# Optimization experiments

Hardware: AMD Instinct MI355X
Metric: run time of the kernel (lower is better)

Reference implementation:

```python
import jax, jax.numpy as jnp
import numpy as np

NUM_HEADS = 16
KERNEL_SIZE = 13  # odd, neighborhood size nh = 6


def setup_inputs() -> dict:
    key = jax.random.key(0)
    ks = jax.random.split(key, 6)
    B, L, C = 4, 4096, 512
    return {
        "x": jax.random.normal(ks[0], (B, L, C), dtype=jnp.float32),
        "qkv_w": jax.random.normal(ks[1], (3 * C, C), dtype=jnp.float32) * (C ** -0.5),
        "qkv_b": jax.random.normal(ks[2], (3 * C,), dtype=jnp.float32) * 0.02,
        "rpb": jax.random.normal(ks[3], (NUM_HEADS, 2 * KERNEL_SIZE - 1), dtype=jnp.float32) * 0.02,
        "proj_w": jax.random.normal(ks[4], (C, C), dtype=jnp.float32) * (C ** -0.5),
        "proj_b": jax.random.normal(ks[5], (C,), dtype=jnp.float32) * 0.02,
    }


def reference(x, qkv_w, qkv_b, rpb, proj_w, proj_b):
    B, L, C = x.shape
    H, K = NUM_HEADS, KERNEL_SIZE
    Dh = C // H
    scale = Dh ** -0.5
    nh = K // 2

    # qkv projection (torch Linear: x @ W.T + b)
    qkv = (x @ qkv_w.T + qkv_b).reshape(B, L, 3, H, Dh)
    qkv = jnp.transpose(qkv, (2, 0, 3, 1, 4))  # (3, B, H, L, Dh)
    q, k, v = qkv[0] * scale, qkv[1], qkv[2]

    # neighborhood indices: window of K keys, shifted (not clipped) at borders
    pos = jnp.arange(L)
    start = jnp.clip(pos - nh, 0, L - K)            # (L,)
    idx = start[:, None] + jnp.arange(K)[None, :]   # (L, K) key positions
    # relative-position-bias index: (key_pos - query_pos) + (K-1), in [0, 2K-2]
    bias_idx = idx - pos[:, None] + (K - 1)         # (L, K)

    k_g = k[:, :, idx, :]                           # (B, H, L, K, Dh)
    attn = jnp.einsum('bhld,bhlkd->bhlk', q, k_g)   # (B, H, L, K)
    attn = attn + rpb[:, bias_idx][None]            # add (H, L, K) bias
    attn = jax.nn.softmax(attn, axis=-1)

    v_g = v[:, :, idx, :]                           # (B, H, L, K, Dh)
    out = jnp.einsum('bhlk,bhlkd->bhld', attn, v_g)  # (B, H, L, Dh)
    out = jnp.transpose(out, (0, 2, 1, 3)).reshape(B, L, C)
    return out @ proj_w.T + proj_b
```

## Files before the change

### kernel.cpp

```cpp
#include <hip/hip_runtime.h>
#include <hip/hip_bf16.h>

#define BATCH   4
#define LSEQ    4096
#define CCH     512
#define HNUM    16
#define DH      32
#define KSZ     13
#define NHALF   6
#define M_TOT   16384
#define N_QKV   1536
#define KDIM    512
#define BK      64

typedef __attribute__((ext_vector_type(8))) short  short8;
typedef __attribute__((ext_vector_type(4))) short  short4_t;
typedef __attribute__((ext_vector_type(4))) float  float4_t;

__device__ __forceinline__ unsigned short f32_to_bf16(float f) {
    union { float f; unsigned int u; } un; un.f = f;
    unsigned int u = un.u;
    u += 0x7FFFu + ((u >> 16) & 1u);
    return (unsigned short)(u >> 16);
}
__device__ __forceinline__ float bf16_to_f32(unsigned short h) {
    union { unsigned int u; float f; } un; un.u = ((unsigned int)h) << 16;
    return un.f;
}

__device__ __forceinline__ void gload_lds16(const unsigned short* g, unsigned short* l) {
    __builtin_amdgcn_global_load_lds(
        (const __attribute__((address_space(1))) unsigned int*)g,
        (__attribute__((address_space(3))) unsigned int*)l,
        16, 0, 0);
}

__global__ void cvt_f32_bf16_v4(const float4_t* __restrict__ in,
                                short4_t* __restrict__ out, int n4) {
    int i = blockIdx.x * blockDim.x + threadIdx.x;
    int stride = gridDim.x * blockDim.x;
    for (; i < n4; i += stride) {
        float4_t v = in[i];
        short4_t h;
        h.x = (short)f32_to_bf16(v.x);
        h.y = (short)f32_to_bf16(v.y);
        h.z = (short)f32_to_bf16(v.z);
        h.w = (short)f32_to_bf16(v.w);
        out[i] = h;
    }
}

__global__ __launch_bounds__(256) void gemm_qkv(
    const unsigned short* __restrict__ Xb,
    const unsigned short* __restrict__ W,
    const float* __restrict__ bias,
    unsigned short* __restrict__ qkvout)
{
    __shared__ __align__(16) unsigned short As[128 * BK];
    __shared__ __align__(16) unsigned short Bs[128 * BK];
    const int tid  = threadIdx.x;
    const int wv   = tid >> 6, ln = tid & 63;
    const int m0   = blockIdx.x * 128;
    const int n0   = blockIdx.y * 128;
    const int wm   = (wv >> 1) * 64;
    const int wn   = (wv & 1) * 64;
    const int lr   = ln & 15;
    const int lg   = ln >> 4;
    const int rgrp = ln >> 3;
    const int csw  = ((ln & 7) ^ rgrp) * 8;

    float4_t acc[4][4];
    #pragma unroll
    for (int m = 0; m < 4; ++m)
        #pragma unroll
        for (int n = 0; n < 4; ++n)
            acc[m][n] = (float4_t){0.f, 0.f, 0.f, 0.f};

    for (int k0 = 0; k0 < KDIM; k0 += BK) {
        #pragma unroll
        for (int it = 0; it < 4; ++it) {
            int ch  = it * 4 + wv;
            int row = ch * 8 + rgrp;
            gload_lds16(Xb + (size_t)(m0 + row) * KDIM + k0 + csw,
                        &As[ch * 8 * BK]);
            gload_lds16(W  + (size_t)(n0 + row) * KDIM + k0 + csw,
                        &Bs[ch * 8 * BK]);
        }
        __syncthreads();
        short8 af[2][4], bfr[2][4];
        #pragma unroll
        for (int kk = 0; kk < 2; ++kk) {
            #pragma unroll
            for (int m = 0; m < 4; ++m) {
                int row = wm + m * 16 + lr;
                int c   = (kk * 4 + lg) ^ (row & 7);
                af[kk][m] = *reinterpret_cast<const short8*>(&As[row * BK + c * 8]);
            }
            #pragma unroll
            for (int n = 0; n < 4; ++n) {
                int row = wn + n * 16 + lr;
                int c   = (kk * 4 + lg) ^ (row & 7);
                bfr[kk][n] = *reinterpret_cast<const short8*>(&Bs[row * BK + c * 8]);
            }
        }
        #pragma unroll
        for (int kk = 0; kk < 2; ++kk)
            #pragma unroll
            for (int m = 0; m < 4; ++m)
                #pragma unroll
                for (int n = 0; n < 4; ++n)
                    acc[m][n] = __builtin_amdgcn_mfma_f32_16x16x32_bf16(
                        af[kk][m], bfr[kk][n], acc[m][n], 0, 0, 0);
        __syncthreads();
    }

    const float qscale = 0.17677669529663687f;
    #pragma unroll
    for (int m = 0; m < 4; ++m) {
        #pragma unroll
        for (int n = 0; n < 4; ++n) {
            int gn    = n0 + wn + n * 16 + lr;
            int which = gn >> 9;
            int hh    = (gn >> 5) & 15;
            int dd    = gn & 31;
            float bsv = bias[gn];
            #pragma unroll
            for (int r = 0; r < 4; ++r) {
                int gm = m0 + wm + m * 16 + lg * 4 + r;
                float v = acc[m][n][r] + bsv;
                if (which == 0) v *= qscale;
                int b_ = gm >> 12, l = gm & 4095;
                size_t off = (((size_t)which * BATCH + b_) * HNUM + hh) *
                                 ((size_t)LSEQ * DH) + (size_t)l * DH + dd;
                qkvout[off] = f32_to_bf16(v);
            }
        }
    }
}

__global__ __launch_bounds__(256) void natten_fwd(
    const unsigned short* __restrict__ qkv,
    const float* __restrict__ rpb,
    unsigned short* __restrict__ ctx)
{
    __shared__ unsigned short ks[268 * DH];
    __shared__ unsigned short vs[268 * DH];
    __shared__ float rpb_s[2 * KSZ - 1];

    const int t    = threadIdx.x;
    const int lblk = blockIdx.x & 15;
    const int bh   = blockIdx.x >> 4;
    const int hh   = bh & 15, b_ = bh >> 4;
    const int l0   = lblk * 256;

    const int r0    = max(l0 - NHALF, 0);
    const int rend  = min(l0 + 256 + NHALF, LSEQ);
    const int nrows = rend - r0;

    const size_t plane = (size_t)LSEQ * DH;
    const size_t kbase = (((size_t)1 * BATCH + b_) * HNUM + hh) * plane;
    const size_t vbase = (((size_t)2 * BATCH + b_) * HNUM + hh) * plane;

    for (int slot = t; slot < nrows * 4; slot += 256) {
        int row = slot >> 2, cq = slot & 3;
        *reinterpret_cast<short8*>(&ks[row * DH + cq * 8]) =
            *reinterpret_cast<const short8*>(&qkv[kbase + (size_t)(r0 + row) * DH + cq * 8]);
        *reinterpret_cast<short8*>(&vs[row * DH + cq * 8]) =
            *reinterpret_cast<const short8*>(&qkv[vbase + (size_t)(r0 + row) * DH + cq * 8]);
    }
    if (t < 2 * KSZ - 1) rpb_s[t] = rpb[hh * (2 * KSZ - 1) + t];
    __syncthreads();

    const int l = l0 + t;
    float q[DH];
    const size_t qoff = (((size_t)0 * BATCH + b_) * HNUM + hh) * plane + (size_t)l * DH;
    #pragma unroll
    for (int cq = 0; cq < 4; ++cq) {
        short8 qv = *reinterpret_cast<const short8*>(&qkv[qoff + cq * 8]);
        #pragma unroll
        for (int e = 0; e < 8; ++e) q[cq * 8 + e] = bf16_to_f32((unsigned short)qv[e]);
    }

    const int start = min(max(l - NHALF, 0), LSEQ - KSZ);
    float logit[KSZ];
    #pragma unroll
    for (int j = 0; j < KSZ; ++j) {
        int kr = start + j - r0;
        float s = 0.f;
        #pragma unroll
        for (int cq = 0; cq < 4; ++cq) {
            short8 kv = *reinterpret_cast<const short8*>(&ks[kr * DH + cq * 8]);
            #pragma unroll
            for (int e = 0; e < 8; ++e)
                s += q[cq * 8 + e] * bf16_to_f32((unsigned short)kv[e]);
        }
        logit[j] = s + rpb_s[start + j - l + (KSZ - 1)];
    }
    float mx = logit[0];
    #pragma unroll
    for (int j = 1; j < KSZ; ++j) mx = fmaxf(mx, logit[j]);
    float p[KSZ], sum = 0.f;
    #pragma unroll
    for (int j = 0; j < KSZ; ++j) { p[j] = __expf(logit[j] - mx); sum += p[j]; }
    const float inv = 1.f / sum;

    float o[DH];
    #pragma unroll
    for (int d = 0; d < DH; ++d) o[d] = 0.f;
    #pragma unroll
    for (int j = 0; j < KSZ; ++j) {
        int kr = start + j - r0;
        float pj = p[j] * inv;
        #pragma unroll
        for (int cq = 0; cq < 4; ++cq) {
            short8 vv = *reinterpret_cast<const short8*>(&vs[kr * DH + cq * 8]);
            #pragma unroll
            for (int e = 0; e < 8; ++e)
                o[cq * 8 + e] += pj * bf16_to_f32((unsigned short)vv[e]);
        }
    }
    const size_t obase = ((size_t)(b_ * LSEQ + l)) * CCH + hh * DH;
    #pragma unroll
    for (int cq = 0; cq < 4; ++cq) {
        short8 ov;
        #pragma unroll
        for (int e = 0; e < 8; ++e) ov[e] = (short)f32_to_bf16(o[cq * 8 + e]);
        *reinterpret_cast<short8*>(&ctx[obase + cq * 8]) = ov;
    }
}

__global__ __launch_bounds__(256) void gemm_proj(
    const unsigned short* __restrict__ Xb,
    const unsigned short* __restrict__ W,
    const float* __restrict__ bias,
    float* __restrict__ out)
{
    __shared__ __align__(16) unsigned short As[128 * BK];
    __shared__ __align__(16) unsigned short Bs[128 * BK];
    const int tid  = threadIdx.x;
    const int wv   = tid >> 6, ln = tid & 63;
    const int m0   = blockIdx.x * 128;
    const int n0   = blockIdx.y * 128;
    const int wm   = (wv >> 1) * 64;
    const int wn   = (wv & 1) * 64;
    const int lr   = ln & 15;
    const int lg   = ln >> 4;
    const int rgrp = ln >> 3;
    const int csw  = ((ln & 7) ^ rgrp) * 8;

    float4_t acc[4][4];
    #pragma unroll
    for (int m = 0; m < 4; ++m)
        #pragma unroll
        for (int n = 0; n < 4; ++n)
            acc[m][n] = (float4_t){0.f, 0.f, 0.f, 0.f};

    for (int k0 = 0; k0 < KDIM; k0 += BK) {
        #pragma unroll
        for (int it = 0; it < 4; ++it) {
            int ch  = it * 4 + wv;
            int row = ch * 8 + rgrp;
            gload_lds16(Xb + (size_t)(m0 + row) * KDIM + k0 + csw,
                        &As[ch * 8 * BK]);
            gload_lds16(W  + (size_t)(n0 + row) * KDIM + k0 + csw,
                        &Bs[ch * 8 * BK]);
        }
        __syncthreads();
        short8 af[2][4], bfr[2][4];
        #pragma unroll
        for (int kk = 0; kk < 2; ++kk) {
            #pragma unroll
            for (int m = 0; m < 4; ++m) {
                int row = wm + m * 16 + lr;
                int c   = (kk * 4 + lg) ^ (row & 7);
                af[kk][m] = *reinterpret_cast<const short8*>(&As[row * BK + c * 8]);
            }
            #pragma unroll
            for (int n = 0; n < 4; ++n) {
                int row = wn + n * 16 + lr;
                int c   = (kk * 4 + lg) ^ (row & 7);
                bfr[kk][n] = *reinterpret_cast<const short8*>(&Bs[row * BK + c * 8]);
            }
        }
        #pragma unroll
        for (int kk = 0; kk < 2; ++kk)
            #pragma unroll
            for (int m = 0; m < 4; ++m)
                #pragma unroll
                for (int n = 0; n < 4; ++n)
                    acc[m][n] = __builtin_amdgcn_mfma_f32_16x16x32_bf16(
                        af[kk][m], bfr[kk][n], acc[m][n], 0, 0, 0);
        __syncthreads();
    }

    #pragma unroll
    for (int m = 0; m < 4; ++m) {
        #pragma unroll
        for (int n = 0; n < 4; ++n) {
            int gn = n0 + wn + n * 16 + lr;
            float bsv = bias[gn];
            #pragma unroll
            for (int r = 0; r < 4; ++r) {
                int gm = m0 + wm + m * 16 + lg * 4 + r;
                out[(size_t)gm * CCH + gn] = acc[m][n][r] + bsv;
            }
        }
    }
}

extern "C" void kernel_launch(void* const* d_in, const int* in_sizes, int n_in,
                              void* d_out, int out_size, void* d_ws, size_t ws_size,
                              hipStream_t stream) {
    const float* x      = (const float*)d_in[0];
    const float* qkv_w  = (const float*)d_in[1];
    const float* qkv_b  = (const float*)d_in[2];
    const float* rpb    = (const float*)d_in[3];
    const float* proj_w = (const float*)d_in[4];
    const float* proj_b = (const float*)d_in[5];
    float* out = (float*)d_out;
    char* ws = (char*)d_ws;

    unsigned short* qkv = (unsigned short*)(ws);
    unsigned short* xb  = (unsigned short*)(ws + 50331648);
    unsigned short* ctx = (unsigned short*)(ws + 50331648);
    unsigned short* wq  = (unsigned short*)(ws + 67108864);
    unsigned short* wp  = (unsigned short*)(ws + 68681728);

    cvt_f32_bf16_v4<<<2048, 256, 0, stream>>>((const float4_t*)x, (short4_t*)xb, M_TOT * KDIM / 4);
    cvt_f32_bf16_v4<<<768, 256, 0, stream>>>((const float4_t*)qkv_w, (short4_t*)wq, 786432 / 4);
    cvt_f32_bf16_v4<<<256, 256, 0, stream>>>((const float4_t*)proj_w, (short4_t*)wp, 262144 / 4);

    dim3 g1(M_TOT / 128, N_QKV / 128);
    gemm_qkv<<<g1, 256, 0, stream>>>(xb, wq, qkv_b, qkv);

    natten_fwd<<<BATCH * HNUM * (LSEQ / 256), 256, 0, stream>>>(qkv, rpb, ctx);

    dim3 g2(M_TOT / 128, CCH / 128);
    gemm_proj<<<g2, 256, 0, stream>>>(ctx, wp, proj_b, out);
}
```

Before: 88.17 us.

## Merge bf16 conversions, use 2-wave GEMM tiles, and split natten LDS by channel quarter

The three fp32-to-bf16 conversion launches are merged into one kernel that handles x and both weight matrices, saving launch overhead. Both GEMMs move from 4 waves with 64x64 warp tiles to 2 waves with 64x128 warp tiles in a 128-thread block, so each wave does more MFMAs per LDS fragment read, at the cost of twice the accumulator registers and possibly lower occupancy. The natten kernel stores K/V in shared memory as four channel-quarter planes instead of row-major, aiming to cut LDS bank conflicts when neighbouring threads read adjacent rows.

```diff
diff --git a/kernel.cpp b/kernel.cpp
--- a/kernel.cpp
+++ b/kernel.cpp
@@ -35,22 +35,28 @@
         16, 0, 0);
 }
 
-__global__ void cvt_f32_bf16_v4(const float4_t* __restrict__ in,
-                                short4_t* __restrict__ out, int n4) {
+__global__ void cvt_all(const float4_t* __restrict__ xin,  short4_t* __restrict__ xo,  int nx,
+                        const float4_t* __restrict__ w1in, short4_t* __restrict__ w1o, int n1,
+                        const float4_t* __restrict__ w2in, short4_t* __restrict__ w2o, int n2) {
     int i = blockIdx.x * blockDim.x + threadIdx.x;
     int stride = gridDim.x * blockDim.x;
-    for (; i < n4; i += stride) {
-        float4_t v = in[i];
+    int ntot = nx + n1 + n2;
+    for (; i < ntot; i += stride) {
+        const float4_t* src; short4_t* dst; int j;
+        if (i < nx)            { src = xin;  dst = xo;  j = i; }
+        else if (i < nx + n1)  { src = w1in; dst = w1o; j = i - nx; }
+        else                   { src = w2in; dst = w2o; j = i - nx - n1; }
+        float4_t v = src[j];
         short4_t h;
         h.x = (short)f32_to_bf16(v.x);
         h.y = (short)f32_to_bf16(v.y);
         h.z = (short)f32_to_bf16(v.z);
         h.w = (short)f32_to_bf16(v.w);
-        out[i] = h;
-    }
-}
-
-__global__ __launch_bounds__(256) void gemm_qkv(
+        dst[j] = h;
+    }
+}
+
+__global__ __launch_bounds__(128) void gemm_qkv(
     const unsigned short* __restrict__ Xb,
     const unsigned short* __restrict__ W,
     const float* __restrict__ bias,
@@ -62,24 +68,23 @@
     const int wv   = tid >> 6, ln = tid & 63;
     const int m0   = blockIdx.x * 128;
     const int n0   = blockIdx.y * 128;
-    const int wm   = (wv >> 1) * 64;
-    const int wn   = (wv & 1) * 64;
+    const int wrow = wv * 64;
     const int lr   = ln & 15;
     const int lg   = ln >> 4;
     const int rgrp = ln >> 3;
     const int csw  = ((ln & 7) ^ rgrp) * 8;
 
-    float4_t acc[4][4];
+    float4_t acc[4][8];
     #pragma unroll
     for (int m = 0; m < 4; ++m)
         #pragma unroll
-        for (int n = 0; n < 4; ++n)
+        for (int n = 0; n < 8; ++n)
             acc[m][n] = (float4_t){0.f, 0.f, 0.f, 0.f};
 
     for (int k0 = 0; k0 < KDIM; k0 += BK) {
         #pragma unroll
-        for (int it = 0; it < 4; ++it) {
-            int ch  = it * 4 + wv;
+        for (int it = 0; it < 8; ++it) {
+            int ch  = it * 2 + wv;
             int row = ch * 8 + rgrp;
             gload_lds16(Xb + (size_t)(m0 + row) * KDIM + k0 + csw,
                         &As[ch * 8 * BK]);
@@ -87,19 +92,19 @@
                         &Bs[ch * 8 * BK]);
         }
         __syncthreads();
-        short8 af[2][4], bfr[2][4];
+        short8 af[2][4], bfr[2][8];
         #pragma unroll
         for (int kk = 0; kk < 2; ++kk) {
             #pragma unroll
             for (int m = 0; m < 4; ++m) {
-                int row = wm + m * 16 + lr;
-                int c   = (kk * 4 + lg) ^ (row & 7);
+                int row = wrow + m * 16 + lr;
+                int c   = (kk * 4 + lg) ^ (lr & 7);
                 af[kk][m] = *reinterpret_cast<const short8*>(&As[row * BK + c * 8]);
             }
             #pragma unroll
-            for (int n = 0; n < 4; ++n) {
-                int row = wn + n * 16 + lr;
-                int c   = (kk * 4 + lg) ^ (row & 7);
+            for (int n = 0; n < 8; ++n) {
+                int row = n * 16 + lr;
+                int c   = (kk * 4 + lg) ^ (lr & 7);
                 bfr[kk][n] = *reinterpret_cast<const short8*>(&Bs[row * BK + c * 8]);
             }
         }
@@ -108,7 +113,7 @@
             #pragma unroll
             for (int m = 0; m < 4; ++m)
                 #pragma unroll
-                for (int n = 0; n < 4; ++n)
+                for (int n = 0; n < 8; ++n)
                     acc[m][n] = __builtin_amdgcn_mfma_f32_16x16x32_bf16(
                         af[kk][m], bfr[kk][n], acc[m][n], 0, 0, 0);
         __syncthreads();
@@ -116,18 +121,18 @@
 
     const float qscale = 0.17677669529663687f;
     #pragma unroll
-    for (int m = 0; m < 4; ++m) {
-        #pragma unroll
-        for (int n = 0; n < 4; ++n) {
-            int gn    = n0 + wn + n * 16 + lr;
+    for (int mf = 0; mf < 4; ++mf) {
+        #pragma unroll
+        for (int nf = 0; nf < 8; ++nf) {
+            int gn    = n0 + nf * 16 + lr;
             int which = gn >> 9;
             int hh    = (gn >> 5) & 15;
             int dd    = gn & 31;
             float bsv = bias[gn];
             #pragma unroll
             for (int r = 0; r < 4; ++r) {
-                int gm = m0 + wm + m * 16 + lg * 4 + r;
-                float v = acc[m][n][r] + bsv;
+                int gm = m0 + wrow + mf * 16 + lg * 4 + r;
+                float v = acc[mf][nf][r] + bsv;
                 if (which == 0) v *= qscale;
                 int b_ = gm >> 12, l = gm & 4095;
                 size_t off = (((size_t)which * BATCH + b_) * HNUM + hh) *
@@ -143,8 +148,8 @@
     const float* __restrict__ rpb,
     unsigned short* __restrict__ ctx)
 {
-    __shared__ unsigned short ks[268 * DH];
-    __shared__ unsigned short vs[268 * DH];
+    __shared__ __align__(16) unsigned short ks[4 * 268 * 8];
+    __shared__ __align__(16) unsigned short vs[4 * 268 * 8];
     __shared__ float rpb_s[2 * KSZ - 1];
 
     const int t    = threadIdx.x;
@@ -161,12 +166,19 @@
     const size_t kbase = (((size_t)1 * BATCH + b_) * HNUM + hh) * plane;
     const size_t vbase = (((size_t)2 * BATCH + b_) * HNUM + hh) * plane;
 
-    for (int slot = t; slot < nrows * 4; slot += 256) {
-        int row = slot >> 2, cq = slot & 3;
-        *reinterpret_cast<short8*>(&ks[row * DH + cq * 8]) =
-            *reinterpret_cast<const short8*>(&qkv[kbase + (size_t)(r0 + row) * DH + cq * 8]);
-        *reinterpret_cast<short8*>(&vs[row * DH + cq * 8]) =
-            *reinterpret_cast<const short8*>(&qkv[vbase + (size_t)(r0 + row) * DH + cq * 8]);
+    {
+        const int cq  = t >> 6;
+        const int rr  = t & 63;
+        #pragma unroll
+        for (int base = 0; base < 320; base += 64) {
+            int row = base + rr;
+            if (row < nrows) {
+                *reinterpret_cast<short8*>(&ks[(cq * 268 + row) * 8]) =
+                    *reinterpret_cast<const short8*>(&qkv[kbase + (size_t)(r0 + row) * DH + cq * 8]);
+                *reinterpret_cast<short8*>(&vs[(cq * 268 + row) * 8]) =
+                    *reinterpret_cast<const short8*>(&qkv[vbase + (size_t)(r0 + row) * DH + cq * 8]);
+            }
+        }
     }
     if (t < 2 * KSZ - 1) rpb_s[t] = rpb[hh * (2 * KSZ - 1) + t];
     __syncthreads();
@@ -189,7 +201,7 @@
         float s = 0.f;
         #pragma unroll
         for (int cq = 0; cq < 4; ++cq) {
-            short8 kv = *reinterpret_cast<const short8*>(&ks[kr * DH + cq * 8]);
+            short8 kv = *reinterpret_cast<const short8*>(&ks[(cq * 268 + kr) * 8]);
             #pragma unroll
             for (int e = 0; e < 8; ++e)
                 s += q[cq * 8 + e] * bf16_to_f32((unsigned short)kv[e]);
@@ -213,7 +225,7 @@
         float pj = p[j] * inv;
         #pragma unroll
         for (int cq = 0; cq < 4; ++cq) {
-            short8 vv = *reinterpret_cast<const short8*>(&vs[kr * DH + cq * 8]);
+            short8 vv = *reinterpret_cast<const short8*>(&vs[(cq * 268 + kr) * 8]);
             #pragma unroll
             for (int e = 0; e < 8; ++e)
                 o[cq * 8 + e] += pj * bf16_to_f32((unsigned short)vv[e]);
@@ -229,7 +241,7 @@
     }
 }
 
-__global__ __launch_bounds__(256) void gemm_proj(
+__global__ __launch_bounds__(128) void gemm_proj(
     const unsigned short* __restrict__ Xb,
     const unsigned short* __restrict__ W,
     const float* __restrict__ bias,
@@ -241,24 +253,23 @@
     const int wv   = tid >> 6, ln = tid & 63;
     const int m0   = blockIdx.x * 128;
     const int n0   = blockIdx.y * 128;
-    const int wm   = (wv >> 1) * 64;
-    const int wn   = (wv & 1) * 64;
+    const int wrow = wv * 64;
     const int lr   = ln & 15;
     const int lg   = ln >> 4;
     const int rgrp = ln >> 3;
     const int csw  = ((ln & 7) ^ rgrp) * 8;
 
-    float4_t acc[4][4];
+    float4_t acc[4][8];
     #pragma unroll
     for (int m = 0; m < 4; ++m)
         #pragma unroll
-        for (int n = 0; n < 4; ++n)
+        for (int n = 0; n < 8; ++n)
             acc[m][n] = (float4_t){0.f, 0.f, 0.f, 0.f};
 
     for (int k0 = 0; k0 < KDIM; k0 += BK) {
         #pragma unroll
-        for (int it = 0; it < 4; ++it) {
-            int ch  = it * 4 + wv;
+        for (int it = 0; it < 8; ++it) {
+            int ch  = it * 2 + wv;
             int row = ch * 8 + rgrp;
             gload_lds16(Xb + (size_t)(m0 + row) * KDIM + k0 + csw,
                         &As[ch * 8 * BK]);
@@ -266,19 +277,19 @@
                         &Bs[ch * 8 * BK]);
         }
         __syncthreads();
-        short8 af[2][4], bfr[2][4];
+        short8 af[2][4], bfr[2][8];
         #pragma unroll
         for (int kk = 0; kk < 2; ++kk) {
             #pragma unroll
             for (int m = 0; m < 4; ++m) {
-                int row = wm + m * 16 + lr;
-                int c   = (kk * 4 + lg) ^ (row & 7);
+                int row = wrow + m * 16 + lr;
+                int c   = (kk * 4 + lg) ^ (lr & 7);
                 af[kk][m] = *reinterpret_cast<const short8*>(&As[row * BK + c * 8]);
             }
             #pragma unroll
-            for (int n = 0; n < 4; ++n) {
-                int row = wn + n * 16 + lr;
-                int c   = (kk * 4 + lg) ^ (row & 7);
+            for (int n = 0; n < 8; ++n) {
+                int row = n * 16 + lr;
+                int c   = (kk * 4 + lg) ^ (lr & 7);
                 bfr[kk][n] = *reinterpret_cast<const short8*>(&Bs[row * BK + c * 8]);
             }
         }
@@ -287,22 +298,22 @@
             #pragma unroll
             for (int m = 0; m < 4; ++m)
                 #pragma unroll
-                for (int n = 0; n < 4; ++n)
+                for (int n = 0; n < 8; ++n)
                     acc[m][n] = __builtin_amdgcn_mfma_f32_16x16x32_bf16(
                         af[kk][m], bfr[kk][n], acc[m][n], 0, 0, 0);
         __syncthreads();
     }
 
     #pragma unroll
-    for (int m = 0; m < 4; ++m) {
-        #pragma unroll
-        for (int n = 0; n < 4; ++n) {
-            int gn = n0 + wn + n * 16 + lr;
+    for (int mf = 0; mf < 4; ++mf) {
+        #pragma unroll
+        for (int nf = 0; nf < 8; ++nf) {
+            int gn = n0 + nf * 16 + lr;
             float bsv = bias[gn];
             #pragma unroll
             for (int r = 0; r < 4; ++r) {
-                int gm = m0 + wm + m * 16 + lg * 4 + r;
-                out[(size_t)gm * CCH + gn] = acc[m][n][r] + bsv;
+                int gm = m0 + wrow + mf * 16 + lg * 4 + r;
+                out[(size_t)gm * CCH + gn] = acc[mf][nf][r] + bsv;
             }
         }
     }
@@ -326,15 +337,16 @@
     unsigned short* wq  = (unsigned short*)(ws + 67108864);
     unsigned short* wp  = (unsigned short*)(ws + 68681728);
 
-    cvt_f32_bf16_v4<<<2048, 256, 0, stream>>>((const float4_t*)x, (short4_t*)xb, M_TOT * KDIM / 4);
-    cvt_f32_bf16_v4<<<768, 256, 0, stream>>>((const float4_t*)qkv_w, (short4_t*)wq, 786432 / 4);
-    cvt_f32_bf16_v4<<<256, 256, 0, stream>>>((const float4_t*)proj_w, (short4_t*)wp, 262144 / 4);
+    cvt_all<<<2048, 256, 0, stream>>>(
+        (const float4_t*)x,      (short4_t*)xb, M_TOT * KDIM / 4,
+        (const float4_t*)qkv_w,  (short4_t*)wq, 786432 / 4,
+        (const float4_t*)proj_w, (short4_t*)wp, 262144 / 4);
 
     dim3 g1(M_TOT / 128, N_QKV / 128);
-    gemm_qkv<<<g1, 256, 0, stream>>>(xb, wq, qkv_b, qkv);
+    gemm_qkv<<<g1, 128, 0, stream>>>(xb, wq, qkv_b, qkv);
 
     natten_fwd<<<BATCH * HNUM * (LSEQ / 256), 256, 0, stream>>>(qkv, rpb, ctx);
 
     dim3 g2(M_TOT / 128, CCH / 128);
-    gemm_proj<<<g2, 256, 0, stream>>>(ctx, wp, proj_b, out);
-}
+    gemm_proj<<<g2, 128, 0, stream>>>(ctx, wp, proj_b, out);
+}
```

Result: slower. 101.8 us (+15.4%).

## Fuse bf16 conversions, remap GEMM blocks across XCDs, split NATTEN LDS by chunk

Applied to the files above, without the earlier changes.

The three f32-to-bf16 conversion launches become one grid-stride kernel covering x and both weight matrices. Both GEMMs switch to a 1D grid with a block-index remap that puts each group of eight consecutive workgroups, which the hardware likely spreads across the chips, on contiguous M tiles for better cache locality. The NATTEN kernel stores K and V in LDS as separate 8-element chunk planes, so lanes reading neighbouring rows hit different banks instead of a 64-byte stride. Together these aim to cut launch overhead, L2 misses and LDS bank conflicts, at the cost of extra index arithmetic and branching in the conversion loop.

```diff
diff --git a/kernel.cpp b/kernel.cpp
--- a/kernel.cpp
+++ b/kernel.cpp
@@ -35,18 +35,24 @@
         16, 0, 0);
 }
 
-__global__ void cvt_f32_bf16_v4(const float4_t* __restrict__ in,
-                                short4_t* __restrict__ out, int n4) {
+__global__ void cvt_all(const float4_t* __restrict__ xin,  short4_t* __restrict__ xo,  int nx,
+                        const float4_t* __restrict__ w1in, short4_t* __restrict__ w1o, int n1,
+                        const float4_t* __restrict__ w2in, short4_t* __restrict__ w2o, int n2) {
     int i = blockIdx.x * blockDim.x + threadIdx.x;
     int stride = gridDim.x * blockDim.x;
-    for (; i < n4; i += stride) {
-        float4_t v = in[i];
+    int ntot = nx + n1 + n2;
+    for (; i < ntot; i += stride) {
+        const float4_t* src; short4_t* dst; int j;
+        if (i < nx)            { src = xin;  dst = xo;  j = i; }
+        else if (i < nx + n1)  { src = w1in; dst = w1o; j = i - nx; }
+        else                   { src = w2in; dst = w2o; j = i - nx - n1; }
+        float4_t v = src[j];
         short4_t h;
         h.x = (short)f32_to_bf16(v.x);
         h.y = (short)f32_to_bf16(v.y);
         h.z = (short)f32_to_bf16(v.z);
         h.w = (short)f32_to_bf16(v.w);
-        out[i] = h;
+        dst[j] = h;
     }
 }
 
@@ -60,8 +66,12 @@
     __shared__ __align__(16) unsigned short Bs[128 * BK];
     const int tid  = threadIdx.x;
     const int wv   = tid >> 6, ln = tid & 63;
-    const int m0   = blockIdx.x * 128;
-    const int n0   = blockIdx.y * 128;
+
+    const int wg   = blockIdx.x;
+    const int wgid = (wg & 7) * 192 + (wg >> 3);
+    const int m0   = (wgid & 127) * 128;
+    const int n0   = (wgid >> 7) * 128;
+
     const int wm   = (wv >> 1) * 64;
     const int wn   = (wv & 1) * 64;
     const int lr   = ln & 15;
@@ -143,8 +153,8 @@
     const float* __restrict__ rpb,
     unsigned short* __restrict__ ctx)
 {
-    __shared__ unsigned short ks[268 * DH];
-    __shared__ unsigned short vs[268 * DH];
+    __shared__ __align__(16) unsigned short ks[4 * 268 * 8];
+    __shared__ __align__(16) unsigned short vs[4 * 268 * 8];
     __shared__ float rpb_s[2 * KSZ - 1];
 
     const int t    = threadIdx.x;
@@ -161,12 +171,19 @@
     const size_t kbase = (((size_t)1 * BATCH + b_) * HNUM + hh) * plane;
     const size_t vbase = (((size_t)2 * BATCH + b_) * HNUM + hh) * plane;
 
-    for (int slot = t; slot < nrows * 4; slot += 256) {
-        int row = slot >> 2, cq = slot & 3;
-        *reinterpret_cast<short8*>(&ks[row * DH + cq * 8]) =
-            *reinterpret_cast<const short8*>(&qkv[kbase + (size_t)(r0 + row) * DH + cq * 8]);
-        *reinterpret_cast<short8*>(&vs[row * DH + cq * 8]) =
-            *reinterpret_cast<const short8*>(&qkv[vbase + (size_t)(r0 + row) * DH + cq * 8]);
+    {
+        const int cq  = t >> 6;
+        const int rr  = t & 63;
+        #pragma unroll
+        for (int base = 0; base < 320; base += 64) {
+            int row = base + rr;
+            if (row < nrows) {
+                *reinterpret_cast<short8*>(&ks[(cq * 268 + row) * 8]) =
+                    *reinterpret_cast<const short8*>(&qkv[kbase + (size_t)(r0 + row) * DH + cq * 8]);
+                *reinterpret_cast<short8*>(&vs[(cq * 268 + row) * 8]) =
+                    *reinterpret_cast<const short8*>(&qkv[vbase + (size_t)(r0 + row) * DH + cq * 8]);
+            }
+        }
     }
     if (t < 2 * KSZ - 1) rpb_s[t] = rpb[hh * (2 * KSZ - 1) + t];
     __syncthreads();
@@ -189,7 +206,7 @@
         float s = 0.f;
         #pragma unroll
         for (int cq = 0; cq < 4; ++cq) {
-            short8 kv = *reinterpret_cast<const short8*>(&ks[kr * DH + cq * 8]);
+            short8 kv = *reinterpret_cast<const short8*>(&ks[(cq * 268 + kr) * 8]);
             #pragma unroll
             for (int e = 0; e < 8; ++e)
                 s += q[cq * 8 + e] * bf16_to_f32((unsigned short)kv[e]);
@@ -213,7 +230,7 @@
         float pj = p[j] * inv;
         #pragma unroll
         for (int cq = 0; cq < 4; ++cq) {
-            short8 vv = *reinterpret_cast<const short8*>(&vs[kr * DH + cq * 8]);
+            short8 vv = *reinterpret_cast<const short8*>(&vs[(cq * 268 + kr) * 8]);
             #pragma unroll
             for (int e = 0; e < 8; ++e)
                 o[cq * 8 + e] += pj * bf16_to_f32((unsigned short)vv[e]);
@@ -239,8 +256,12 @@
     __shared__ __align__(16) unsigned short Bs[128 * BK];
     const int tid  = threadIdx.x;
     const int wv   = tid >> 6, ln = tid & 63;
-    const int m0   = blockIdx.x * 128;
-    const int n0   = blockIdx.y * 128;
+
+    const int wg   = blockIdx.x;
+    const int wgid = (wg & 7) * 64 + (wg >> 3);
+    const int m0   = (wgid & 127) * 128;
+    const int n0   = (wgid >> 7) * 128;
+
     const int wm   = (wv >> 1) * 64;
     const int wn   = (wv & 1) * 64;
     const int lr   = ln & 15;
@@ -326,15 +347,14 @@
     unsigned short* wq  = (unsigned short*)(ws + 67108864);
     unsigned short* wp  = (unsigned short*)(ws + 68681728);
 
-    cvt_f32_bf16_v4<<<2048, 256, 0, stream>>>((const float4_t*)x, (short4_t*)xb, M_TOT * KDIM / 4);
-    cvt_f32_bf16_v4<<<768, 256, 0, stream>>>((const float4_t*)qkv_w, (short4_t*)wq, 786432 / 4);
-    cvt_f32_bf16_v4<<<256, 256, 0, stream>>>((const float4_t*)proj_w, (short4_t*)wp, 262144 / 4);
-
-    dim3 g1(M_TOT / 128, N_QKV / 128);
-    gemm_qkv<<<g1, 256, 0, stream>>>(xb, wq, qkv_b, qkv);
+    cvt_all<<<2048, 256, 0, stream>>>(
+        (const float4_t*)x,      (short4_t*)xb, M_TOT * KDIM / 4,
+        (const float4_t*)qkv_w,  (short4_t*)wq, 786432 / 4,
+        (const float4_t*)proj_w, (short4_t*)wp, 262144 / 4);
+
+    gemm_qkv<<<1536, 256, 0, stream>>>(xb, wq, qkv_b, qkv);
 
     natten_fwd<<<BATCH * HNUM * (LSEQ / 256), 256, 0, stream>>>(qkv, rpb, ctx);
 
-    dim3 g2(M_TOT / 128, CCH / 128);
-    gemm_proj<<<g2, 256, 0, stream>>>(ctx, wp, proj_b, out);
-}
+    gemm_proj<<<512, 256, 0, stream>>>(ctx, wp, proj_b, out);
+}
```

New measurement: 93.70 us. 1.06x slower.
